# Optimization experiments

Hardware: AMD Instinct MI355X
Metric: run time of the kernel (lower is better)

Reference implementation:

```python
import jax, jax.numpy as jnp
import numpy as np

IN_F = 2
DIM_H = 64
DT = 0.02          # step_size
INTENSITY = 40.0   # Poisson rate multiplier
RATE = jnp.array([10.0, 1.0], dtype=jnp.float32)  # Gamma rates per feature


def _xavier(key, fan_in, fan_out):
    lim = float(np.sqrt(6.0 / (fan_in + fan_out)))
    return jax.random.uniform(key, (fan_in, fan_out), minval=-lim, maxval=lim, dtype=jnp.float32)


def setup_inputs() -> dict:
    key = jax.random.key(0)
    k0, k1, k2 = jax.random.split(key, 3)
    Nsim, steps = 100000, 200
    z0 = jax.random.normal(k0, (Nsim, IN_F), dtype=jnp.float32)
    W1 = _xavier(k1, IN_F, DIM_H)
    b1 = jnp.zeros((DIM_H,), dtype=jnp.float32)
    W2 = _xavier(k2, DIM_H, IN_F)
    b2 = jnp.zeros((IN_F,), dtype=jnp.float32)
    diffusion = jnp.float32(1.0)
    return {"z0": z0, "W1": W1, "b1": b1, "W2": W2, "b2": b2,
            "diffusion": diffusion, "Nsim": Nsim, "steps": steps}


def _drift(x, W1, b1, W2, b2):
    # MLP: Linear(2,64) -> tanh -> Linear(64,2)
    h = jnp.tanh(x @ W1 + b1)
    return h @ W2 + b2


def reference(z0, W1, b1, W2, b2, diffusion, Nsim, steps):
    sqrt_dt = jnp.float32(np.sqrt(DT))
    n = z0.shape[0]

    def step(state, key):
        kp, kn, kg = jax.random.split(key, 3)
        # Poisson(intensity*dt) jump counts, shape [N,1]
        pois = jax.random.poisson(kp, INTENSITY * DT, (n, 1)).astype(jnp.float32)
        a = jnp.broadcast_to(pois, (n, IN_F))  # Gamma concentration per feature
        # Gamma(conc=pois, rate=RATE); conc==0 -> sample is exactly 0
        g = jax.random.gamma(kg, jnp.maximum(a, 1.0), dtype=jnp.float32) / RATE
        jump = jnp.where(a > 0, g, 0.0)
        noise = jax.random.normal(kn, (n, IN_F), dtype=jnp.float32)
        new_state = (state
                     + _drift(state, W1, b1, W2, b2) * DT
                     + diffusion * sqrt_dt * noise
                     + jump)
        return new_state, new_state

    keys = jax.random.split(jax.random.key(42), steps)
    _, path = jax.lax.scan(step, z0, keys)            # [steps, N, F]
    path = jnp.concatenate([z0[None], path], axis=0)   # [steps+1, N, F]
    return jnp.transpose(path, (1, 0, 2))              # [N, steps+1, F]
```

## Files before the change

kernel.cpp:

```cpp
#include <hip/hip_runtime.h>
#include <cstdint>
#include <cmath>

#define DEVINL __device__ __forceinline__

struct U2 { uint32_t a, b; };

DEVINL uint32_t rotl32(uint32_t x, uint32_t r){ return (x << r) | (x >> (32u - r)); }

DEVINL U2 tf(uint32_t k0, uint32_t k1, uint32_t x0, uint32_t x1){
  const uint32_t k2 = k0 ^ k1 ^ 0x1BD11BDAu;
  x0 += k0; x1 += k1;
#define TFR(r) { x0 += x1; x1 = rotl32(x1,(r)); x1 ^= x0; }
  TFR(13) TFR(15) TFR(26) TFR(6)  x0 += k1; x1 += k2 + 1u;
  TFR(17) TFR(29) TFR(16) TFR(24) x0 += k2; x1 += k0 + 2u;
  TFR(13) TFR(15) TFR(26) TFR(6)  x0 += k0; x1 += k1 + 3u;
  TFR(17) TFR(29) TFR(16) TFR(24) x0 += k1; x1 += k2 + 4u;
  TFR(13) TFR(15) TFR(26) TFR(6)  x0 += k2; x1 += k0 + 5u;
#undef TFR
  U2 r; r.a = x0; r.b = x1; return r;
}

DEVINL uint32_t pbits(uint32_t k0, uint32_t k1, uint32_t idx){
  U2 r = tf(k0, k1, 0u, idx);
  return r.a ^ r.b;
}

DEVINL float u01(uint32_t bits){
  return __uint_as_float((bits >> 9) | 0x3F800000u) - 1.0f;
}

DEVINL float xla_logf(float xin){
  float xf = fmaxf(__uint_as_float(0x00800000u), xin);
  uint32_t ib = __float_as_uint(xf);
  float e = (float)((int)(ib >> 23) - 126);
  float x = __uint_as_float((ib & 0x807fffffu) | 0x3f000000u);
  bool m = x < 0.707106781186547524f;
  float t = m ? x : 0.0f;
  x = __fsub_rn(x, 1.0f);
  if (m) e = __fsub_rn(e, 1.0f);
  x = __fadd_rn(x, t);
  float z = __fmul_rn(x, x);
  float y = 7.0376836292e-2f;
  y = fmaf(y, x, -1.1514610310e-1f);
  y = fmaf(y, x,  1.1676998740e-1f);
  y = fmaf(y, x, -1.2420140846e-1f);
  y = fmaf(y, x,  1.4249322787e-1f);
  y = fmaf(y, x, -1.6668057665e-1f);
  y = fmaf(y, x,  2.0000714765e-1f);
  y = fmaf(y, x, -2.4999993993e-1f);
  y = fmaf(y, x,  3.3333331174e-1f);
  y = __fmul_rn(y, x);
  y = __fmul_rn(y, z);
  y = fmaf(e, -2.12194440e-4f, y);
  y = fmaf(z, -0.5f, y);
  x = __fadd_rn(x, y);
  x = fmaf(e, 0.693359375f, x);
  if (xin == 0.0f) x = __uint_as_float(0xff800000u);
  return x;
}

DEVINL float xla_log1pf(float v){
  float av = fabsf(v);
  if (av < 1e-4f) return __fmul_rn(__fadd_rn(__fmul_rn(-0.5f, v), 1.0f), v);
  return xla_logf(__fadd_rn(v, 1.0f));
}

DEVINL float erfinv32(float x){
  float xx = __fmul_rn(x, x);
  float w = -xla_log1pf(-xx);
  float p;
  if (w < 5.0f){
    float ww = __fsub_rn(w, 2.5f);
    p = 2.81022636e-08f;
    p = __fadd_rn( 3.43273939e-07f, __fmul_rn(p, ww));
    p = __fadd_rn(-3.5233877e-06f,  __fmul_rn(p, ww));
    p = __fadd_rn(-4.39150654e-06f, __fmul_rn(p, ww));
    p = __fadd_rn( 0.00021858087f,  __fmul_rn(p, ww));
    p = __fadd_rn(-0.00125372503f,  __fmul_rn(p, ww));
    p = __fadd_rn(-0.00417768164f,  __fmul_rn(p, ww));
    p = __fadd_rn( 0.246640727f,    __fmul_rn(p, ww));
    p = __fadd_rn( 1.50140941f,     __fmul_rn(p, ww));
  } else {
    float ww = __fsub_rn(sqrtf(w), 3.0f);
    p = -0.000200214257f;
    p = __fadd_rn( 0.000100950558f, __fmul_rn(p, ww));
    p = __fadd_rn( 0.00134934322f,  __fmul_rn(p, ww));
    p = __fadd_rn(-0.00367342844f,  __fmul_rn(p, ww));
    p = __fadd_rn( 0.00573950773f,  __fmul_rn(p, ww));
    p = __fadd_rn(-0.0076224613f,   __fmul_rn(p, ww));
    p = __fadd_rn( 0.00943887047f,  __fmul_rn(p, ww));
    p = __fadd_rn( 1.00167406f,     __fmul_rn(p, ww));
    p = __fadd_rn( 2.83297682f,     __fmul_rn(p, ww));
  }
  return __fmul_rn(p, x);
}

#define SQRT2F (__uint_as_float(0x3FB504F3u))
#define NLOF   (__uint_as_float(0xBF7FFFFFu))

DEVINL float normal_from_bits(uint32_t bits){
  float ff = u01(bits);
  float u = __fadd_rn(__fmul_rn(ff, 2.0f), NLOF);
  u = fmaxf(NLOF, u);
  return __fmul_rn(SQRT2F, erfinv32(u));
}

DEVINL float fast_tanh(float x){
  float ax = fabsf(x);
  float e = __expf(-2.0f * ax);
  float r = (1.0f - e) * __builtin_amdgcn_rcpf(1.0f + e);
  return __builtin_copysignf(r, x);
}

DEVINL float gamma_one(uint32_t gk0, uint32_t gk1, float alpha){
  const float d = __fsub_rn(alpha, (1.0f/3.0f));
  const float c = (1.0f/3.0f) / sqrtf(d);
  U2 K = tf(gk0, gk1, 0u, 0u);
  for (;;) {
    U2 xk = tf(K.a, K.b, 0u, 1u);
    U2 Uk = tf(K.a, K.b, 0u, 2u);
    float xx, v;
    for (;;) {
      U2 sub = tf(xk.a, xk.b, 0u, 1u);
      uint32_t nb = pbits(sub.a, sub.b, 0u);
      xx = normal_from_bits(nb);
      v = __fadd_rn(1.0f, __fmul_rn(xx, c));
      if (v > 0.0f) break;
      xk = tf(xk.a, xk.b, 0u, 0u);
    }
    float X = __fmul_rn(xx, xx);
    float V = __fmul_rn(__fmul_rn(v, v), v);
    float U = u01(pbits(Uk.a, Uk.b, 0u));
    float sq = __fsub_rn(1.0f, __fmul_rn(0.0331f, __fmul_rn(X, X)));
    if (U < sq) return __fmul_rn(d, V);
    float lnU = xla_logf(U);
    float lnV = xla_logf(V);
    float rhs = __fadd_rn(__fmul_rn(X, 0.5f),
                          __fmul_rn(d, __fadd_rn(__fsub_rn(1.0f, V), lnV)));
    if (lnU < rhs) return __fmul_rn(d, V);
    K = tf(K.a, K.b, 0u, 0u);
  }
}

#define NPK 24
#define WSTRIDE (4 + 2*NPK)
#define KEYOFF 8
#define JOFF   16384

__global__ void setup_kernel(uint32_t* __restrict__ ws, int steps){
  int t = blockIdx.x * blockDim.x + threadIdx.x;
  if (t >= steps) return;
  U2 kt = tf(0u, 42u, 0u, (uint32_t)t);
  U2 kp = tf(kt.a, kt.b, 0u, 0u);
  U2 kn = tf(kt.a, kt.b, 0u, 1u);
  U2 kg = tf(kt.a, kt.b, 0u, 2u);
  uint32_t* p = ws + KEYOFF + (size_t)t * WSTRIDE;
  p[0] = kn.a; p[1] = kn.b;
  p[2] = kg.a; p[3] = kg.b;
  uint32_t r0 = kp.a, r1 = kp.b;
  for (int i = 0; i < NPK; ++i) {
    U2 sub = tf(r0, r1, 0u, 1u);
    U2 rn  = tf(r0, r1, 0u, 0u);
    p[4 + 2*i] = sub.a; p[5 + 2*i] = sub.b;
    r0 = rn.a; r1 = rn.b;
  }
}

__global__ __launch_bounds__(256) void pois_kernel(
    uint32_t* __restrict__ ws, int N, int steps, uint32_t POFF, uint32_t COFF)
{
  __shared__ uint32_t cnts[4];
  int e = blockIdx.x * 256 + threadIdx.x;
  int t = blockIdx.y;
  bool act = e < N;
  const uint32_t* __restrict__ p = ws + KEYOFF + (size_t)t * WSTRIDE;
  int pois = 0;
  if (act) {
    float lp = 0.0f; int k = 0;
    #pragma unroll 1
    for (int i = 0; i < NPK; ++i) {
      if (!(lp > -0.8f)) break;
      k++;
      uint32_t bits = pbits(p[4 + 2*i], p[5 + 2*i], (uint32_t)e);
      lp = __fadd_rn(lp, xla_logf(u01(bits)));
    }
    pois = k - 1;
    float* jarr = (float*)(ws + JOFF);
    size_t jb = (size_t)t * (size_t)(2*N) + 2u*(uint32_t)e;
    jarr[jb] = 0.0f; jarr[jb + 1] = 0.0f;
    ((uint8_t*)ws)[(size_t)POFF*4u + (size_t)t*(size_t)N + (size_t)e] = (uint8_t)pois;
  }
  uint64_t b = __ballot(act && (pois > 0));
  int lane = threadIdx.x & 63, w = threadIdx.x >> 6;
  if (lane == 0) cnts[w] = (uint32_t)__popcll(b);
  __syncthreads();
  if (threadIdx.x == 0)
    ws[COFF + (size_t)blockIdx.y * gridDim.x + blockIdx.x] =
        cnts[0] + cnts[1] + cnts[2] + cnts[3];
}

__global__ __launch_bounds__(256) void prefix_kernel(
    uint32_t* __restrict__ ws, uint32_t COFF, uint32_t BOFF, int NB)
{
  __shared__ uint32_t ssum[256];
  int i = threadIdx.x;
  int chunk = (NB + 255) >> 8;
  int lo = i * chunk, hi = lo + chunk; if (hi > NB) hi = NB;
  uint32_t s = 0;
  for (int j = lo; j < hi; ++j) s += ws[COFF + j];
  ssum[i] = s;
  __syncthreads();
  if (i == 0) {
    uint32_t run = 0;
    for (int k = 0; k < 256; ++k) { uint32_t c = ssum[k]; ssum[k] = run; run += c; }
    ws[0] = run;
  }
  __syncthreads();
  uint32_t base = ssum[i];
  for (int j = lo; j < hi; ++j) { ws[BOFF + j] = base; base += ws[COFF + j]; }
}

__global__ __launch_bounds__(256) void scatter_kernel(
    uint32_t* __restrict__ ws, int N, int steps,
    uint32_t POFF, uint32_t BOFF, uint32_t WOFF, uint32_t CAP)
{
  __shared__ uint32_t cnts[4];
  int e = blockIdx.x * 256 + threadIdx.x;
  int t = blockIdx.y;
  bool act = e < N;
  uint32_t pv = 0;
  if (act) pv = ((const uint8_t*)ws)[(size_t)POFF*4u + (size_t)t*(size_t)N + (size_t)e];
  uint64_t b = __ballot(pv > 0);
  int lane = threadIdx.x & 63, w = threadIdx.x >> 6;
  if (lane == 0) cnts[w] = (uint32_t)__popcll(b);
  __syncthreads();
  uint32_t bid = (uint32_t)blockIdx.y * gridDim.x + blockIdx.x;
  uint32_t wb = ws[BOFF + bid];
  for (int w2 = 0; w2 < w; ++w2) wb += cnts[w2];
  if (pv > 0) {
    uint32_t rank = (uint32_t)__popcll(b & ((1ull << lane) - 1ull));
    uint32_t idx = wb + rank;
    if (idx < CAP)
      ws[WOFF + idx] = ((uint32_t)t << 23) | ((uint32_t)e << 6) | pv;
  }
}

__global__ __launch_bounds__(256) void gamma_kernel(
    uint32_t* __restrict__ ws, int N, uint32_t WOFF, uint32_t CAP)
{
  uint32_t total = ws[0]; if (total > CAP) total = CAP;
  uint32_t j = blockIdx.x * 256u + threadIdx.x;
  if (j >= 2u * total) return;
  uint32_t ent = ws[WOFF + (j >> 1)];
  uint32_t t = ent >> 23, e = (ent >> 6) & 0x1FFFFu, pv = ent & 0x3Fu;
  const uint32_t* __restrict__ p = ws + KEYOFF + (size_t)t * WSTRIDE;
  uint32_t f = j & 1u;
  U2 gk = tf(p[2], p[3], 0u, 2u*e + f);
  float s = gamma_one(gk.a, gk.b, (float)pv);
  float* jarr = (float*)(ws + JOFF);
  jarr[(size_t)t * (size_t)(2*N) + (size_t)(2u*e + f)] = f ? s : (s / 10.0f);
}

__global__ __launch_bounds__(256) void jump_kernel(
    uint32_t* __restrict__ ws, int N, int steps)
{
  int e = blockIdx.x * 256 + threadIdx.x;
  int t = blockIdx.y;
  if (e >= N) return;
  const uint32_t* __restrict__ p = ws + KEYOFF + (size_t)t * WSTRIDE;
  const uint32_t ue = (uint32_t)e;
  float lp = 0.0f; int k = 0;
  #pragma unroll 1
  for (int i = 0; i < NPK; ++i) {
    if (!(lp > -0.8f)) break;
    k++;
    uint32_t bits = pbits(p[4 + 2*i], p[5 + 2*i], ue);
    lp = __fadd_rn(lp, xla_logf(u01(bits)));
  }
  int pois = k - 1;
  float* jarr = (float*)(ws + JOFF);
  size_t jbase = (size_t)t * (size_t)(2*N) + (size_t)(2*e);
  float j0 = 0.0f, j1 = 0.0f;
  if (pois > 0) {
    uint32_t kg0 = p[2], kg1 = p[3];
    float alpha = (float)pois;
    U2 gk0 = tf(kg0, kg1, 0u, 2u*ue);
    j0 = gamma_one(gk0.a, gk0.b, alpha) / 10.0f;
    U2 gk1 = tf(kg0, kg1, 0u, 2u*ue + 1u);
    j1 = gamma_one(gk1.a, gk1.b, alpha);
  }
  jarr[jbase] = j0; jarr[jbase + 1] = j1;
}

#define IBLK 64
__global__ __launch_bounds__(IBLK) void integrate_kernel(
    const float* __restrict__ z0, const float* __restrict__ W1,
    const float* __restrict__ b1, const float* __restrict__ W2,
    const float* __restrict__ b2, const float* __restrict__ diffp,
    const uint32_t* __restrict__ ws, float* __restrict__ out,
    int N, int steps)
{
  __shared__ float smem[322 + IBLK*9];
  for (int k = threadIdx.x; k < 322; k += IBLK) {
    float v;
    if (k < 128)      v = W1[k];
    else if (k < 192) v = b1[k - 128];
    else if (k < 320) v = W2[k - 192];
    else              v = b2[k - 320];
    smem[k] = v;
  }
  __syncthreads();
  const float* sW1 = smem;
  const float* sb1 = smem + 128;
  const float* sW2 = smem + 192;
  const float* sb2 = smem + 320;
  float* sx = smem + 322;

  const int lane = threadIdx.x;
  const int tid  = blockIdx.x * IBLK + lane;
  const bool act = tid < 2 * N;
  const int elemBase = blockIdx.x * 32;
  if (elemBase >= N) return;
  const int e = tid >> 1;
  const int f = tid & 1;
  const uint32_t utid = (uint32_t)tid;

  float x = act ? z0[tid] : 0.0f;
  const size_t orow = (size_t)(steps + 1) * 2u;
  if (act) out[(size_t)e * orow + (size_t)f] = x;

  const float DTf  = 0.02f;
  const float sqdt = (float)0.14142135623730951;
  const float coef = __fmul_rn(diffp[0], sqdt);
  const int   hbase = f << 5;
  const float* __restrict__ jarr = (const float*)(ws + JOFF);
  const int m = lane & 15, g = lane >> 4;

  for (int t = 0; t < steps; ++t) {
    const uint32_t* __restrict__ p = ws + KEYOFF + (size_t)t * WSTRIDE;

    float jump = act ? jarr[(size_t)t * (size_t)(2*N) + utid] : 0.0f;
    float nf = normal_from_bits(pbits(p[0], p[1], utid));

    float xo = __shfl_xor(x, 1, 64);
    float xf0 = (f == 0) ? x : xo;
    float xf1 = (f == 0) ? xo : x;
    float p0 = 0.0f, p1 = 0.0f;
    #pragma unroll
    for (int i = 0; i < 32; ++i) {
      int h = hbase + i;
      float hv = fast_tanh(fmaf(xf0, sW1[h], fmaf(xf1, sW1[64 + h], sb1[h])));
      p0 = fmaf(hv, sW2[2*h],     p0);
      p1 = fmaf(hv, sW2[2*h + 1], p1);
    }
    float q0 = p0 + __shfl_xor(p0, 1, 64);
    float q1 = p1 + __shfl_xor(p1, 1, 64);
    float dr = sb2[f] + ((f == 0) ? q0 : q1);

    x = __fadd_rn(__fadd_rn(__fadd_rn(x, __fmul_rn(dr, DTf)),
                            __fmul_rn(coef, nf)), jump);
    sx[lane*9 + (t & 7)] = x;
    if ((t & 7) == 7) {
      #pragma unroll
      for (int i = 0; i < 8; ++i) {
        int el = 4*i + g;
        float v = sx[(2*el + (m & 1))*9 + (m >> 1)];
        int elem = elemBase + el;
        if (elem < N)
          out[(size_t)elem * orow + (size_t)((t - 6)*2 + m)] = v;
      }
    }
  }
  int rem = steps & 7;
  if (rem) {
    int T0 = steps - rem;
    #pragma unroll
    for (int i = 0; i < 8; ++i) {
      int el = 4*i + g;
      if ((m >> 1) < rem) {
        float v = sx[(2*el + (m & 1))*9 + (m >> 1)];
        int elem = elemBase + el;
        if (elem < N)
          out[(size_t)elem * orow + (size_t)((T0 + 1)*2 + m)] = v;
      }
    }
  }
}

__global__ __launch_bounds__(64) void sim_fallback_kernel(
    const float* __restrict__ z0, const float* __restrict__ W1,
    const float* __restrict__ b1, const float* __restrict__ W2,
    const float* __restrict__ b2, const float* __restrict__ diffp,
    const uint32_t* __restrict__ ws, float* __restrict__ out,
    int N, int steps)
{
  __shared__ float smem[322];
  for (int k = threadIdx.x; k < 322; k += 64) {
    float v;
    if (k < 128)      v = W1[k];
    else if (k < 192) v = b1[k - 128];
    else if (k < 320) v = W2[k - 192];
    else              v = b2[k - 320];
    smem[k] = v;
  }
  __syncthreads();
  const float* sW1 = smem;
  const float* sb1 = smem + 128;
  const float* sW2 = smem + 192;
  const float* sb2 = smem + 320;

  int tid = blockIdx.x * 64 + threadIdx.x;
  if (tid >= 2 * N) return;
  const int e = tid >> 1;
  const int f = tid & 1;
  const uint32_t ue   = (uint32_t)e;
  const uint32_t utid = (uint32_t)tid;

  float x = z0[tid];
  const size_t obase = (size_t)e * (size_t)(steps + 1) * 2u + (size_t)f;
  out[obase] = x;

  const float DTf  = 0.02f;
  const float sqdt = (float)0.14142135623730951;
  const float coef = __fmul_rn(diffp[0], sqdt);
  const int   hbase = f << 5;

  for (int t = 0; t < steps; ++t) {
    const uint32_t* __restrict__ p = ws + KEYOFF + (size_t)t * WSTRIDE;
    int pois;
    {
      float lp = 0.0f;
      pois = NPK - 1;
      #pragma unroll 1
      for (int m = 0; m < NPK/2; ++m) {
        int i0 = 2*m + f;
        uint32_t bits = pbits(p[4 + 2*i0], p[5 + 2*i0], ue);
        float lmine = xla_logf(u01(bits));
        float lother = __shfl_xor(lmine, 1, 64);
        float la = (f == 0) ? lmine : lother;
        float lb = (f == 0) ? lother : lmine;
        float s1 = __fadd_rn(lp, la);
        float s2 = __fadd_rn(s1, lb);
        if (!(s1 > -0.8f)) { pois = 2*m; break; }
        if (!(s2 > -0.8f)) { pois = 2*m + 1; break; }
        lp = s2;
      }
    }
    float nf = normal_from_bits(pbits(p[0], p[1], utid));
    float jump = 0.0f;
    if (pois > 0) {
      U2 gk = tf(p[2], p[3], 0u, utid);
      float s = gamma_one(gk.a, gk.b, (float)pois);
      jump = (f == 0) ? (s / 10.0f) : s;
    }
    float xo = __shfl_xor(x, 1, 64);
    float xf0 = (f == 0) ? x : xo;
    float xf1 = (f == 0) ? xo : x;
    float p0 = 0.0f, p1 = 0.0f;
    #pragma unroll
    for (int i = 0; i < 32; ++i) {
      int h = hbase + i;
      float hv = fast_tanh(fmaf(xf0, sW1[h], fmaf(xf1, sW1[64 + h], sb1[h])));
      p0 = fmaf(hv, sW2[2*h],     p0);
      p1 = fmaf(hv, sW2[2*h + 1], p1);
    }
    float q0 = p0 + __shfl_xor(p0, 1, 64);
    float q1 = p1 + __shfl_xor(p1, 1, 64);
    float dr = sb2[f] + ((f == 0) ? q0 : q1);
    x = __fadd_rn(__fadd_rn(__fadd_rn(x, __fmul_rn(dr, DTf)),
                            __fmul_rn(coef, nf)), jump);
    out[obase + (size_t)(t + 1) * 2u] = x;
  }
}

extern "C" void kernel_launch(void* const* d_in, const int* in_sizes, int n_in,
                              void* d_out, int out_size, void* d_ws, size_t ws_size,
                              hipStream_t stream) {
  const float* z0  = (const float*)d_in[0];
  const float* W1  = (const float*)d_in[1];
  const float* b1  = (const float*)d_in[2];
  const float* W2  = (const float*)d_in[3];
  const float* b2  = (const float*)d_in[4];
  const float* dif = (const float*)d_in[5];
  int N = in_sizes[0] / 2;
  int steps = out_size / (N * 2) - 1;
  uint32_t* ws = (uint32_t*)d_ws;
  int total = 2 * N;

  hipLaunchKernelGGL(setup_kernel, dim3((steps + 255) / 256), dim3(256), 0, stream,
                     ws, steps);

  size_t JSZ = (size_t)2 * (size_t)N * (size_t)steps;
  size_t PSZ = ((size_t)N * (size_t)steps + 3u) / 4u;
  int    NBX = (N + 255) / 256;
  size_t NB  = (size_t)NBX * (size_t)steps;
  size_t CAP = ((size_t)N * (size_t)steps * 11u) / 16u;
  size_t POFFs = (size_t)JOFF + JSZ;
  size_t COFFs = POFFs + PSZ;
  size_t BOFFs = COFFs + NB;
  size_t WOFFs = BOFFs + NB;
  size_t need0 = (WOFFs + CAP) * 4u;
  size_t need1 = ((size_t)JOFF + JSZ) * 4u;
  bool pk = (N < (1 << 17)) && (steps < (1 << 9)) && (steps <= 314) &&
            (WOFFs + CAP < 0xFFFFFFFFull);

  if (pk && ws_size >= need0) {
    hipLaunchKernelGGL(pois_kernel, dim3(NBX, steps), dim3(256), 0, stream,
                       ws, N, steps, (uint32_t)POFFs, (uint32_t)COFFs);
    hipLaunchKernelGGL(prefix_kernel, dim3(1), dim3(256), 0, stream,
                       ws, (uint32_t)COFFs, (uint32_t)BOFFs, (int)NB);
    hipLaunchKernelGGL(scatter_kernel, dim3(NBX, steps), dim3(256), 0, stream,
                       ws, N, steps, (uint32_t)POFFs, (uint32_t)BOFFs,
                       (uint32_t)WOFFs, (uint32_t)CAP);
    size_t gth = 2u * CAP;
    hipLaunchKernelGGL(gamma_kernel, dim3((gth + 255) / 256), dim3(256), 0, stream,
                       ws, N, (uint32_t)WOFFs, (uint32_t)CAP);
    hipLaunchKernelGGL(integrate_kernel, dim3((total + IBLK - 1) / IBLK), dim3(IBLK),
                       0, stream, z0, W1, b1, W2, b2, dif, ws, (float*)d_out, N, steps);
  } else if (steps <= 314 && ws_size >= need1) {
    hipLaunchKernelGGL(jump_kernel, dim3((N + 255) / 256, steps), dim3(256), 0, stream,
                       ws, N, steps);
    hipLaunchKernelGGL(integrate_kernel, dim3((total + IBLK - 1) / IBLK), dim3(IBLK),
                       0, stream, z0, W1, b1, W2, b2, dif, ws, (float*)d_out, N, steps);
  } else {
    hipLaunchKernelGGL(sim_fallback_kernel, dim3((total + 63) / 64), dim3(64), 0, stream,
                       z0, W1, b1, W2, b2, dif, ws, (float*)d_out, N, steps);
  }
}
```

Measured before the change: 1.703 ms.

## Use packed FMA MLP, larger blocks, and direct nontemporal output stores

Replaces the shared-memory transpose staging of output with direct per-step nontemporal stores. It raises the block size from 64 to 256 and rewrites the MLP inner loop with two-wide vector FMAs so the compiler can emit packed fp32 instructions. The aim is to cut LDS staging and barrier-free shuffle overhead and to halve the FMA instruction count. The trade-off is that direct stores are strided by the 402-float row, so each store touches scattered cache lines, which may hurt write coalescing.

```diff
diff --git a/kernel.cpp b/kernel.cpp
--- a/kernel.cpp
+++ b/kernel.cpp
@@ -5,6 +5,7 @@
 #define DEVINL __device__ __forceinline__
 
 struct U2 { uint32_t a, b; };
+typedef float v2f __attribute__((ext_vector_type(2)));
 
 DEVINL uint32_t rotl32(uint32_t x, uint32_t r){ return (x << r) | (x >> (32u - r)); }
 
@@ -113,6 +114,8 @@
   return __builtin_copysignf(r, x);
 }
 
+DEVINL v2f f2fma(v2f a, v2f b, v2f c){ return __builtin_elementwise_fma(a, b, c); }
+
 DEVINL float gamma_one(uint32_t gk0, uint32_t gk1, float alpha){
   const float d = __fsub_rn(alpha, (1.0f/3.0f));
   const float c = (1.0f/3.0f) / sqrtf(d);
@@ -293,7 +296,7 @@
   jarr[jbase] = j0; jarr[jbase + 1] = j1;
 }
 
-#define IBLK 64
+#define IBLK 256
 __global__ __launch_bounds__(IBLK) void integrate_kernel(
     const float* __restrict__ z0, const float* __restrict__ W1,
     const float* __restrict__ b1, const float* __restrict__ W2,
@@ -301,7 +304,7 @@
     const uint32_t* __restrict__ ws, float* __restrict__ out,
     int N, int steps)
 {
-  __shared__ float smem[322 + IBLK*9];
+  __shared__ float smem[322];
   for (int k = threadIdx.x; k < 322; k += IBLK) {
     float v;
     if (k < 128)      v = W1[k];
@@ -315,76 +318,57 @@
   const float* sb1 = smem + 128;
   const float* sW2 = smem + 192;
   const float* sb2 = smem + 320;
-  float* sx = smem + 322;
-
-  const int lane = threadIdx.x;
-  const int tid  = blockIdx.x * IBLK + lane;
-  const bool act = tid < 2 * N;
-  const int elemBase = blockIdx.x * 32;
-  if (elemBase >= N) return;
+
+  int tid = blockIdx.x * IBLK + threadIdx.x;
+  if (tid >= 2 * N) return;
   const int e = tid >> 1;
   const int f = tid & 1;
   const uint32_t utid = (uint32_t)tid;
 
-  float x = act ? z0[tid] : 0.0f;
-  const size_t orow = (size_t)(steps + 1) * 2u;
-  if (act) out[(size_t)e * orow + (size_t)f] = x;
+  float x = z0[tid];
+  const size_t obase = (size_t)e * (size_t)(steps + 1) * 2u + (size_t)f;
+  __builtin_nontemporal_store(x, &out[obase]);
 
   const float DTf  = 0.02f;
   const float sqdt = (float)0.14142135623730951;
   const float coef = __fmul_rn(diffp[0], sqdt);
   const int   hbase = f << 5;
   const float* __restrict__ jarr = (const float*)(ws + JOFF);
-  const int m = lane & 15, g = lane >> 4;
 
   for (int t = 0; t < steps; ++t) {
     const uint32_t* __restrict__ p = ws + KEYOFF + (size_t)t * WSTRIDE;
 
-    float jump = act ? jarr[(size_t)t * (size_t)(2*N) + utid] : 0.0f;
+    float jump = jarr[(size_t)t * (size_t)(2*N) + utid];
+
     float nf = normal_from_bits(pbits(p[0], p[1], utid));
 
     float xo = __shfl_xor(x, 1, 64);
     float xf0 = (f == 0) ? x : xo;
     float xf1 = (f == 0) ? xo : x;
-    float p0 = 0.0f, p1 = 0.0f;
+    v2f xv0 = (v2f){xf0, xf0};
+    v2f xv1 = (v2f){xf1, xf1};
+    v2f acc = (v2f){0.0f, 0.0f};
     #pragma unroll
-    for (int i = 0; i < 32; ++i) {
-      int h = hbase + i;
-      float hv = fast_tanh(fmaf(xf0, sW1[h], fmaf(xf1, sW1[64 + h], sb1[h])));
-      p0 = fmaf(hv, sW2[2*h],     p0);
-      p1 = fmaf(hv, sW2[2*h + 1], p1);
+    for (int j = 0; j < 16; ++j) {
+      int h = hbase + 2*j;
+      v2f w1lo = *(const v2f*)&sW1[h];
+      v2f w1hi = *(const v2f*)&sW1[64 + h];
+      v2f b1v  = *(const v2f*)&sb1[h];
+      v2f pre  = f2fma(xv0, w1lo, f2fma(xv1, w1hi, b1v));
+      float hv0 = fast_tanh(pre.x);
+      float hv1 = fast_tanh(pre.y);
+      v2f w2a = *(const v2f*)&sW2[2*h];
+      v2f w2b = *(const v2f*)&sW2[2*h + 2];
+      acc = f2fma((v2f){hv0, hv0}, w2a, acc);
+      acc = f2fma((v2f){hv1, hv1}, w2b, acc);
     }
-    float q0 = p0 + __shfl_xor(p0, 1, 64);
-    float q1 = p1 + __shfl_xor(p1, 1, 64);
+    float q0 = acc.x + __shfl_xor(acc.x, 1, 64);
+    float q1 = acc.y + __shfl_xor(acc.y, 1, 64);
     float dr = sb2[f] + ((f == 0) ? q0 : q1);
 
     x = __fadd_rn(__fadd_rn(__fadd_rn(x, __fmul_rn(dr, DTf)),
                             __fmul_rn(coef, nf)), jump);
-    sx[lane*9 + (t & 7)] = x;
-    if ((t & 7) == 7) {
-      #pragma unroll
-      for (int i = 0; i < 8; ++i) {
-        int el = 4*i + g;
-        float v = sx[(2*el + (m & 1))*9 + (m >> 1)];
-        int elem = elemBase + el;
-        if (elem < N)
-          out[(size_t)elem * orow + (size_t)((t - 6)*2 + m)] = v;
-      }
-    }
-  }
-  int rem = steps & 7;
-  if (rem) {
-    int T0 = steps - rem;
-    #pragma unroll
-    for (int i = 0; i < 8; ++i) {
-      int el = 4*i + g;
-      if ((m >> 1) < rem) {
-        float v = sx[(2*el + (m & 1))*9 + (m >> 1)];
-        int elem = elemBase + el;
-        if (elem < N)
-          out[(size_t)elem * orow + (size_t)((T0 + 1)*2 + m)] = v;
-      }
-    }
+    __builtin_nontemporal_store(x, &out[obase + (size_t)(t + 1) * 2u]);
   }
 }
 
```

Result: slower. 2.155 ms (+26.5%).
